# Kernel optimization log

Measured on AMD Instinct MI355X. Metric: run time of the kernel, lower is better.

Reference implementation:

```python
import jax, jax.numpy as jnp
import numpy as np
import math

HIDDEN = 2048
NUM_HEADS = 16
NUM_KV_HEADS = 4
HEAD_DIM = 128
GROUPS = NUM_HEADS // NUM_KV_HEADS
BATCH = 1
SEQ = 4096
THETA = 10000.0


def _rope(x):
    # x: [B, h, S, D], interleaved-pair rotation as in the torch module
    seq = x.shape[2]
    freqs = 1.0 / (THETA ** (jnp.arange(0, HEAD_DIM, 2, dtype=jnp.float32) / HEAD_DIM))  # [D/2]
    angles = jnp.arange(seq, dtype=jnp.float32)[:, None] * freqs[None, :]  # [S, D/2]
    cos = jnp.cos(angles)[None, None]  # [1,1,S,D/2]
    sin = jnp.sin(angles)[None, None]
    x1 = x[..., 0::2]
    x2 = x[..., 1::2]
    # stack along new last axis then flatten -> interleaved layout
    rot = jnp.stack([x1 * cos - x2 * sin, x1 * sin + x2 * cos], axis=-1)
    return rot.reshape(x.shape)


def setup_inputs() -> dict:
    key = jax.random.key(0)
    kx, kq, kk, kv, ko = jax.random.split(key, 5)
    scale = 0.02
    x = jax.random.normal(kx, (BATCH, SEQ, HIDDEN), dtype=jnp.float32)
    Wq = jax.random.normal(kq, (NUM_HEADS * HEAD_DIM, HIDDEN), dtype=jnp.float32) * scale
    Wk = jax.random.normal(kk, (NUM_KV_HEADS * HEAD_DIM, HIDDEN), dtype=jnp.float32) * scale
    Wv = jax.random.normal(kv, (NUM_KV_HEADS * HEAD_DIM, HIDDEN), dtype=jnp.float32) * scale
    Wo = jax.random.normal(ko, (HIDDEN, NUM_HEADS * HEAD_DIM), dtype=jnp.float32) * scale
    return {"x": x, "Wq": Wq, "Wk": Wk, "Wv": Wv, "Wo": Wo}


def reference(x, Wq, Wk, Wv, Wo):
    B, S, _ = x.shape
    q = (x @ Wq.T).reshape(B, S, NUM_HEADS, HEAD_DIM).transpose(0, 2, 1, 3)      # [B,16,S,D]
    k = (x @ Wk.T).reshape(B, S, NUM_KV_HEADS, HEAD_DIM).transpose(0, 2, 1, 3)   # [B,4,S,D]
    v = (x @ Wv.T).reshape(B, S, NUM_KV_HEADS, HEAD_DIM).transpose(0, 2, 1, 3)
    q = _rope(q)
    k = _rope(k)
    # GQA: repeat_interleave KV heads across the group dim
    k = jnp.repeat(k, GROUPS, axis=1)  # [B,16,S,D]
    v = jnp.repeat(v, GROUPS, axis=1)
    scale = 1.0 / math.sqrt(HEAD_DIM)
    scores = jnp.einsum("bhqd,bhkd->bhqk", q, k) * scale  # [B,16,S,S]
    causal = jnp.triu(jnp.ones((S, S), dtype=bool), k=1)
    scores = jnp.where(causal[None, None], jnp.float32(-jnp.inf), scores)
    attn = jax.nn.softmax(scores, axis=-1)
    out = jnp.einsum("bhqk,bhkd->bhqd", attn, v)           # [B,16,S,D]
    out = out.transpose(0, 2, 1, 3).reshape(B, S, NUM_HEADS * HEAD_DIM)
    return out @ Wo.T
```

## Files before the change

kernel.cpp:

```cpp
#include <hip/hip_runtime.h>
#include <hip/hip_bf16.h>

typedef unsigned short u16;
typedef unsigned int u32;
typedef short short8 __attribute__((ext_vector_type(8)));
typedef unsigned short ushort4v __attribute__((ext_vector_type(4)));
typedef float f32x4 __attribute__((ext_vector_type(4)));
typedef float f32x16 __attribute__((ext_vector_type(16)));
typedef u32 u32x4 __attribute__((ext_vector_type(4)));

#define SEQN 4096
#define HID 2048
#define NH 16
#define NKV 4
#define HD 128
#define QDIM 2048
#define KVD 512
#define QKVS 3072

static __device__ __forceinline__ float bf2f(u16 u){
  unsigned x = ((unsigned)u) << 16; float f; __builtin_memcpy(&f, &x, 4); return f;
}
static __device__ __forceinline__ u16 f2bf(float f){
  unsigned x; __builtin_memcpy(&x, &f, 4);
  x += 0x7fffu + ((x >> 16) & 1u);
  return (u16)(x >> 16);
}
static __device__ __forceinline__ u16 f2bfc(float f){
  unsigned x; __builtin_memcpy(&x, &f, 4);
  return (u16)((x + 0x8000u) >> 16);
}
static __device__ __forceinline__ u32 pkr(float a, float b){
  u32 ab, bb; __builtin_memcpy(&ab, &a, 4); __builtin_memcpy(&bb, &b, 4);
  return ((ab + 0x8000u) >> 16) | ((bb + 0x8000u) & 0xffff0000u);
}

#define G1 (SEQN*HID/4)
#define G2 (QDIM*HID/4)
#define G3 (KVD*HID/4)
#define G4 (KVD*HID/4)
#define G5 (HID*QDIM/4)
__global__ __launch_bounds__(256) void cvt5_kernel(const float* __restrict__ x,  const float* __restrict__ Wq,
                                                   const float* __restrict__ Wk, const float* __restrict__ Wv,
                                                   const float* __restrict__ Wo, u16* __restrict__ xb,
                                                   u16* __restrict__ Wqkvb, u16* __restrict__ Wob){
  int g = blockIdx.x * 256 + threadIdx.x;
  const float* src; u16* dst; int off;
  if (g < G1)                { src = x;  dst = xb;    off = g; }
  else if (g < G1+G2)        { src = Wq; dst = Wqkvb; off = g - G1; }
  else if (g < G1+G2+G3)     { src = Wk; dst = Wqkvb + (size_t)QDIM*HID;        off = g - (G1+G2); }
  else if (g < G1+G2+G3+G4)  { src = Wv; dst = Wqkvb + (size_t)(QDIM+KVD)*HID;  off = g - (G1+G2+G3); }
  else if (g < G1+G2+G3+G4+G5){ src = Wo; dst = Wob;  off = g - (G1+G2+G3+G4); }
  else return;
  f32x4 v = ((const f32x4*)src)[off];
  ushort4v o;
  o.x = f2bf(v.x); o.y = f2bf(v.y); o.z = f2bf(v.z); o.w = f2bf(v.w);
  ((ushort4v*)dst)[off] = o;
}

#define ROPE_BLKS (SEQN * (NH + NKV) * 16 / 256)
__global__ __launch_bounds__(256) void prep_kernel(u16* __restrict__ QKVb, u16* __restrict__ VTg){
  __shared__ u16 T[64][72];
  const int bid = blockIdx.x;
  const int tid = threadIdx.x;
  if (bid < ROPE_BLKS){
    int idx = bid * 256 + tid;
    int i8 = idx & 15;
    int rest = idx >> 4;
    int h = rest % (NH + NKV);
    int s = rest / (NH + NKV);
    int col = (h < NH) ? h * HD : QDIM + (h - NH) * HD;
    u16* p = QKVb + (size_t)s * QKVS + col + i8 * 8;
    short8 v = *(const short8*)p;
    short8 o;
#pragma unroll
    for (int j = 0; j < 4; j++){
      int i = i8 * 4 + j;
      float freq = expf(-0.14391156831212788f * (float)i);
      float ang = (float)s * freq;
      float c = cosf(ang), sn = sinf(ang);
      float x1 = bf2f((u16)v[2*j]), x2 = bf2f((u16)v[2*j+1]);
      o[2*j]   = (short)f2bfc(x1 * c - x2 * sn);
      o[2*j+1] = (short)f2bfc(x1 * sn + x2 * c);
    }
    *(short8*)p = o;
  } else {
    const int b2 = bid - ROPE_BLKS;
    const int s0 = (b2 & 63) * 64;
    const int c0 = (b2 >> 6) * 64;
    const int sl = tid & 63, ch = tid >> 6;
    const u16* src = QKVb + QDIM + KVD + (size_t)(s0 + sl) * QKVS + c0 + ch * 16;
    *(short8*)&T[sl][ch * 16]     = *(const short8*)(src);
    *(short8*)&T[sl][ch * 16 + 8] = *(const short8*)(src + 8);
    __syncthreads();
#pragma unroll
    for (int it = 0; it < 16; it++){
      int c = it * 4 + ch;
      VTg[(size_t)(c0 + c) * SEQN + s0 + sl] = T[sl][c];
    }
  }
}

static __device__ __forceinline__ void gload16(const void* g, void* l){
  __builtin_amdgcn_global_load_lds((const __attribute__((address_space(1))) void*)g,
                                   (__attribute__((address_space(3))) void*)l, 16, 0, 0);
}

template<int F32OUT>
__global__ __launch_bounds__(256) void gemm_kernel(const u16* __restrict__ A, const u16* __restrict__ B,
                                                   void* __restrict__ Cout, int M, int N, int Kd, int ldc){
  __shared__ alignas(16) u16 sh[8192];
  u16* As = sh;
  u16* Bs = sh + 4096;
  const int tid = threadIdx.x;
  const int w = tid >> 6, l = tid & 63;
  const int wr = w >> 1, wc = w & 1;
  const int lc = l & 15, lg = l >> 4;
  const int tm = blockIdx.x * 128, tn = blockIdx.y * 128;

  const int srow = w * 32 + (l >> 2);
  const int scol = (l & 3) * 8;
  const u16* Ag = A + (size_t)(tm + srow) * Kd + scol;
  const u16* Bg = B + (size_t)(tn + srow) * Kd + scol;
  u16* As0 = As + (w * 2) * 512;
  u16* Bs0 = Bs + (w * 2) * 512;

  f32x4 acc[4][4] = {};

  for (int k0 = 0; k0 < Kd; k0 += 32){
    gload16(Ag + k0,                    As0);
    gload16(Ag + k0 + (size_t)16 * Kd,  As0 + 512);
    gload16(Bg + k0,                    Bs0);
    gload16(Bg + k0 + (size_t)16 * Kd,  Bs0 + 512);
    __syncthreads();
    short8 a[4], b[4];
#pragma unroll
    for (int mi = 0; mi < 4; mi++) a[mi] = *(const short8*)&As[(wr*64 + mi*16 + lc) * 32 + lg*8];
#pragma unroll
    for (int ni = 0; ni < 4; ni++) b[ni] = *(const short8*)&Bs[(wc*64 + ni*16 + lc) * 32 + lg*8];
#pragma unroll
    for (int mi = 0; mi < 4; mi++)
#pragma unroll
      for (int ni = 0; ni < 4; ni++)
        acc[mi][ni] = __builtin_amdgcn_mfma_f32_16x16x32_bf16(a[mi], b[ni], acc[mi][ni], 0, 0, 0);
    __syncthreads();
  }

  if (F32OUT){
#pragma unroll
    for (int mi = 0; mi < 4; mi++)
#pragma unroll
      for (int ni = 0; ni < 4; ni++)
#pragma unroll
        for (int r = 0; r < 4; r++){
          int row = tm + wr*64 + mi*16 + lg*4 + r;
          int col = tn + wc*64 + ni*16 + lc;
          ((float*)Cout)[(size_t)row * ldc + col] = acc[mi][ni][r];
        }
  } else {
    __syncthreads();
    u16* Ew = sh + w * 1168;
#pragma unroll
    for (int mi = 0; mi < 4; mi++){
#pragma unroll
      for (int ni = 0; ni < 4; ni++)
#pragma unroll
        for (int r = 0; r < 4; r++)
          Ew[(lg * 4 + r) * 73 + ni * 16 + lc] = f2bfc(acc[mi][ni][r]);
#pragma unroll
      for (int pass = 0; pass < 2; pass++){
        int row = pass * 8 + (l >> 3);
        short8 v;
#pragma unroll
        for (int j = 0; j < 8; j++) v[j] = (short)Ew[row * 73 + (l & 7) * 8 + j];
        *(short8*)((u16*)Cout + (size_t)(tm + wr*64 + mi*16 + row) * ldc + tn + wc*64 + (l & 7) * 8) = v;
      }
    }
  }
}

__global__ __launch_bounds__(256, 2) void attn_kernel(const u16* __restrict__ Qg, const u16* __restrict__ Kgb,
                                                      const u16* __restrict__ VTg, u16* __restrict__ Aout,
                                                      u16* __restrict__ PO, float* __restrict__ mP,
                                                      float* __restrict__ LP){
  __shared__ alignas(16) char pool[65536];

  const int pr  = blockIdx.x;
  const int h   = blockIdx.y;
  const int s   = blockIdx.z;
  const int kvh = h >> 2;
  const int tid = threadIdx.x;
  const int w = tid >> 6, l = tid & 63;
  const int q5 = l & 31;
  const int hi = l >> 5;
  const int hi4 = hi * 4;
  const float csc = 0.12751743f;

  const u16* Ksrc[4];
  const u16* Vsrc[4];
#pragma unroll
  for (int i = 0; i < 4; i++){
    int blk = w * 4 + i;
    int row = blk * 4 + (l >> 4);
    int cg  = (l & 15) ^ (row & 15);
    Ksrc[i] = Kgb + (size_t)row * QKVS + kvh * HD + cg * 8;
    int d   = blk * 8 + (l >> 3);
    int cv  = (l & 7) ^ (d & 7);
    Vsrc[i] = VTg + (size_t)(kvh * 128 + d) * SEQN + cv * 8;
  }

  auto issueTile = [&](int b, int kv0){
    char* Ksb = pool + b * 32768;
    char* VTb = Ksb + 16384;
#pragma unroll
    for (int i = 0; i < 4; i++)
      gload16(Ksrc[i] + (size_t)kv0 * QKVS, Ksb + (w * 4 + i) * 1024);
#pragma unroll
    for (int i = 0; i < 4; i++)
      gload16(Vsrc[i] + kv0, VTb + (w * 4 + i) * 1024);
  };

  const int qlo = pr, qhi = 31 - pr;
  int nseg, sq[2], st0[2], st1[2], smode[2];
  if (s == 0){
    nseg = 2;
    sq[0] = qlo; st0[0] = 0;           st1[0] = 2 * pr + 2;   smode[0] = 0;
    sq[1] = qhi; st0[1] = 0;           st1[1] = 31 - 2 * pr;  smode[1] = 1;
  } else {
    nseg = 1;
    sq[0] = qhi; st0[0] = 31 - 2 * pr; st1[0] = 64 - 2 * pr;  smode[0] = 2;
  }

  for (int sg = 0; sg < nseg; sg++){
    const int qt = sq[sg], t0 = st0[sg], t1 = st1[sg], mode = smode[sg];
    const int qbase = qt * 128 + w * 32;
    const int qa    = qbase + q5;

    short8 qf[8];
    {
      const u16* qp = Qg + (size_t)(qbase + q5) * QKVS + h * HD + hi * 8;
#pragma unroll
      for (int k0 = 0; k0 < 8; k0++) qf[k0] = *(const short8*)(qp + k0 * 16);
    }

    f32x16 Ov[4] = {};
    float Lrow = 0.f;
    float ms = -1e30f;

    auto computeTile = [&](int b, int kv0){
      if (kv0 > qbase + 31) return;
      char* Ksb = pool + b * 32768;
      char* VTb = Ksb + 16384;
      f32x16 Sv[2] = {};
#pragma unroll
      for (int k0 = 0; k0 < 8; k0++){
#pragma unroll
        for (int nb = 0; nb < 2; nb++){
          int kvr = nb * 32 + q5;
          short8 kf = *(const short8*)(Ksb + kvr * 256 + (((k0 * 2 + hi) ^ (kvr & 15)) << 4));
          Sv[nb] = __builtin_amdgcn_mfma_f32_32x32x16_bf16(kf, qf[k0], Sv[nb], 0, 0, 0);
        }
      }
      if (kv0 + 63 > qbase){
#pragma unroll
        for (int nb = 0; nb < 2; nb++)
#pragma unroll
          for (int r = 0; r < 16; r++){
            int kva = kv0 + nb * 32 + (r & 3) + 8 * (r >> 2) + hi4;
            if (kva > qa) Sv[nb][r] = -1e30f;
          }
      }
      float tm = fmaxf(Sv[0][0], Sv[0][1]);
#pragma unroll
      for (int nb = 0; nb < 2; nb++)
#pragma unroll
        for (int r = (nb == 0 ? 2 : 0); r < 16; r += 2)
          tm = fmaxf(tm, fmaxf(Sv[nb][r], Sv[nb][r + 1]));
      tm = fmaxf(tm, __shfl_xor(tm, 32));
      float tms = tm * csc;
      if (!__all(tms - ms <= 8.f)){
        float nms = fmaxf(ms, tms);
        float al = __builtin_amdgcn_exp2f(ms - nms);
        ms = nms;
        Lrow *= al;
#pragma unroll
        for (int nb = 0; nb < 4; nb++)
#pragma unroll
          for (int r = 0; r < 16; r++) Ov[nb][r] *= al;
      }
      float ts0 = 0.f, ts1 = 0.f;
#pragma unroll
      for (int nb = 0; nb < 2; nb++)
#pragma unroll
        for (int r = 0; r < 16; r += 2){
          float p0 = __builtin_amdgcn_exp2f(__builtin_fmaf(Sv[nb][r],     csc, -ms));
          float p1 = __builtin_amdgcn_exp2f(__builtin_fmaf(Sv[nb][r + 1], csc, -ms));
          Sv[nb][r] = p0; Sv[nb][r + 1] = p1;
          ts0 += p0; ts1 += p1;
        }
      float ts = ts0 + ts1;
      ts += __shfl_xor(ts, 32);
      Lrow += ts;
#pragma unroll
      for (int kc = 0; kc < 4; kc++){
        const int nb = kc >> 1, rb = (kc & 1) * 8;
        u32 Aw = pkr(Sv[nb][rb + 0], Sv[nb][rb + 1]);
        u32 Bw = pkr(Sv[nb][rb + 2], Sv[nb][rb + 3]);
        u32 Cw = pkr(Sv[nb][rb + 4], Sv[nb][rb + 5]);
        u32 Dw = pkr(Sv[nb][rb + 6], Sv[nb][rb + 7]);
        u32 sAw = __shfl_xor(Aw, 32);
        u32 sBw = __shfl_xor(Bw, 32);
        u32 sCw = __shfl_xor(Cw, 32);
        u32 sDw = __shfl_xor(Dw, 32);
        u32 w0 = hi ? sCw : Aw;
        u32 w1 = hi ? sDw : Bw;
        u32 w2 = hi ? Cw : sAw;
        u32 w3 = hi ? Dw : sBw;
        u32x4 pw4 = {w0, w1, w2, w3};
        short8 pf = *(short8*)&pw4;
#pragma unroll
        for (int nbd = 0; nbd < 4; nbd++){
          int drow = nbd * 32 + q5;
          short8 vf = *(const short8*)(VTb + drow * 128 + (((kc * 2 + hi) ^ (drow & 7)) << 4));
          Ov[nbd] = __builtin_amdgcn_mfma_f32_32x32x16_bf16(vf, pf, Ov[nbd], 0, 0, 0);
        }
      }
    };

    __syncthreads();
    issueTile(0, t0 * 64);
    __syncthreads();
    int cur = 0;
    for (int t = t0; t < t1; t++){
      if (t + 1 < t1) issueTile(cur ^ 1, (t + 1) * 64);
      computeTile(cur, t * 64);
      __syncthreads();
      cur ^= 1;
    }

    u16* Ew = (u16*)(pool + w * 8704);
    float rl = (mode == 0) ? (1.f / Lrow) : 1.f;
#pragma unroll
    for (int nbd = 0; nbd < 4; nbd++)
#pragma unroll
      for (int r = 0; r < 16; r += 2){
        int d = nbd * 32 + (r & 3) + 8 * (r >> 2) + hi4;
        u32 wpk = pkr(Ov[nbd][r] * rl, Ov[nbd][r + 1] * rl);
        *(u32*)((char*)Ew + q5 * 272 + d * 2) = wpk;
      }
    if (mode == 0){
#pragma unroll
      for (int pass = 0; pass < 8; pass++){
        int q2 = pass * 4 + (l >> 4);
        short8 ov = *(const short8*)((char*)Ew + q2 * 272 + (l & 15) * 16);
        *(short8*)(Aout + (size_t)(qbase + q2) * QDIM + h * HD + (l & 15) * 8) = ov;
      }
    } else {
      const int p = mode - 1;
      u16* dstb = PO + ((size_t)((p * 16 + pr) * NH + h) * 128) * 128;
#pragma unroll
      for (int pass = 0; pass < 8; pass++){
        int q2 = pass * 4 + (l >> 4);
        short8 ov = *(const short8*)((char*)Ew + q2 * 272 + (l & 15) * 16);
        *(short8*)(dstb + (size_t)(w * 32 + q2) * 128 + (l & 15) * 8) = ov;
      }
      if (hi == 0){
        int idx = ((p * 16 + pr) * NH + h) * 128 + w * 32 + q5;
        mP[idx] = ms;
        LP[idx] = Lrow;
      }
    }
  }
}

__global__ __launch_bounds__(256) void combine_kernel(const u16* __restrict__ PO, const float* __restrict__ mP,
                                                      const float* __restrict__ LP, u16* __restrict__ Aout){
  const int pr = blockIdx.x;
  const int h  = blockIdx.y;
  const int tid = threadIdx.x;
  const int r  = tid >> 1;
  const int dh = (tid & 1) * 64;
  const int qhi = 31 - pr;
  const int idx0 = ((0 * 16 + pr) * NH + h) * 128 + r;
  const int idx1 = ((1 * 16 + pr) * NH + h) * 128 + r;
  float m0 = mP[idx0], m1 = mP[idx1];
  float L0 = LP[idx0], L1 = LP[idx1];
  float M = fmaxf(m0, m1);
  float a0 = __builtin_amdgcn_exp2f(m0 - M);
  float a1 = __builtin_amdgcn_exp2f(m1 - M);
  float rl = 1.f / (L0 * a0 + L1 * a1);
  const u16* o0 = PO + (size_t)idx0 * 128 + dh;
  const u16* o1 = PO + (size_t)idx1 * 128 + dh;
  u16* dst = Aout + (size_t)(qhi * 128 + r) * QDIM + h * HD + dh;
#pragma unroll
  for (int ch = 0; ch < 8; ch++){
    short8 v0 = *(const short8*)(o0 + ch * 8);
    short8 v1 = *(const short8*)(o1 + ch * 8);
    u32x4 ow;
#pragma unroll
    for (int j = 0; j < 4; j++){
      float e0 = (bf2f((u16)v0[2*j])   * a0 + bf2f((u16)v1[2*j])   * a1) * rl;
      float e1 = (bf2f((u16)v0[2*j+1]) * a0 + bf2f((u16)v1[2*j+1]) * a1) * rl;
      ow[j] = pkr(e0, e1);
    }
    *(u32x4*)(dst + ch * 8) = ow;
  }
}

extern "C" void kernel_launch(void* const* d_in, const int* in_sizes, int n_in,
                              void* d_out, int out_size, void* d_ws, size_t ws_size,
                              hipStream_t stream){
  const float* x  = (const float*)d_in[0];
  const float* Wq = (const float*)d_in[1];
  const float* Wk = (const float*)d_in[2];
  const float* Wv = (const float*)d_in[3];
  const float* Wo = (const float*)d_in[4];

  char* p = (char*)d_ws;
  u16* xb    = (u16*)p; p += (size_t)SEQN * HID * 2;
  u16* Wqkvb = (u16*)p; p += (size_t)QKVS * HID * 2;
  u16* Wob   = (u16*)p; p += (size_t)HID * QDIM * 2;
  u16* QKVb  = (u16*)p; p += (size_t)SEQN * QKVS * 2;
  u16* Ab    = (u16*)p; p += (size_t)SEQN * QDIM * 2;
  u16* VTg   = (u16*)p; p += (size_t)SEQN * KVD * 2;
  u16* PO    = (u16*)p; p += (size_t)2 * 16 * NH * 128 * 128 * 2;
  float* mP  = (float*)p; p += (size_t)2 * 16 * NH * 128 * 4;
  float* LP  = (float*)p; p += (size_t)2 * 16 * NH * 128 * 4;

  const int totg = G1 + G2 + G3 + G4 + G5;
  cvt5_kernel<<<(totg + 255) / 256, 256, 0, stream>>>(x, Wq, Wk, Wv, Wo, xb, Wqkvb, Wob);

  gemm_kernel<0><<<dim3(SEQN/128, QKVS/128), 256, 0, stream>>>(xb, Wqkvb, QKVb, SEQN, QKVS, HID, QKVS);

  prep_kernel<<<ROPE_BLKS + (SEQN/64) * (KVD/64), 256, 0, stream>>>(QKVb, VTg);

  attn_kernel<<<dim3(16, NH, 2), 256, 0, stream>>>(QKVb, QKVb + QDIM, VTg, Ab, PO, mP, LP);
  combine_kernel<<<dim3(16, NH), 256, 0, stream>>>(PO, mP, LP, Ab);

  gemm_kernel<1><<<dim3(SEQN/128, HID/128), 256, 0, stream>>>(Ab, Wob, d_out, SEQN, HID, QDIM, HID);
}
```

Measured before the change: 254.4 us.

## Halve attention KV tile to 32 rows to fit three blocks per CU

Shrinks the K/V tile from 64 to 32 keys, which halves the shared-memory pool and the score registers so the launch bound can go from 2 to 3 blocks per CU. Global source pointers become 32-bit byte offsets to save registers, and the V swizzle and segment tile ranges are rescaled to match. The aim is higher occupancy to hide latency, at the cost of twice as many loop iterations and barriers and more online-softmax rescale checks per key.

```diff
diff --git a/kernel.cpp b/kernel.cpp
--- a/kernel.cpp
+++ b/kernel.cpp
@@ -179,11 +179,11 @@
   }
 }
 
-__global__ __launch_bounds__(256, 2) void attn_kernel(const u16* __restrict__ Qg, const u16* __restrict__ Kgb,
+__global__ __launch_bounds__(256, 3) void attn_kernel(const u16* __restrict__ Qg, const u16* __restrict__ Kgb,
                                                       const u16* __restrict__ VTg, u16* __restrict__ Aout,
                                                       u16* __restrict__ PO, float* __restrict__ mP,
                                                       float* __restrict__ LP){
-  __shared__ alignas(16) char pool[65536];
+  __shared__ alignas(16) char pool[34816];
 
   const int pr  = blockIdx.x;
   const int h   = blockIdx.y;
@@ -196,39 +196,38 @@
   const int hi4 = hi * 4;
   const float csc = 0.12751743f;
 
-  const u16* Ksrc[4];
-  const u16* Vsrc[4];
-#pragma unroll
-  for (int i = 0; i < 4; i++){
-    int blk = w * 4 + i;
+  u32 Koff[2], Voff[2];
+#pragma unroll
+  for (int i = 0; i < 2; i++){
+    int blk = w * 2 + i;
     int row = blk * 4 + (l >> 4);
     int cg  = (l & 15) ^ (row & 15);
-    Ksrc[i] = Kgb + (size_t)row * QKVS + kvh * HD + cg * 8;
-    int d   = blk * 8 + (l >> 3);
-    int cv  = (l & 7) ^ (d & 7);
-    Vsrc[i] = VTg + (size_t)(kvh * 128 + d) * SEQN + cv * 8;
+    Koff[i] = (u32)((row * QKVS + kvh * HD + cg * 8) * 2);
+    int d   = blk * 16 + (l >> 2);
+    int cv  = (l & 3) ^ (d & 3);
+    Voff[i] = (u32)(((kvh * 128 + d) * SEQN + cv * 8) * 2);
   }
 
   auto issueTile = [&](int b, int kv0){
-    char* Ksb = pool + b * 32768;
-    char* VTb = Ksb + 16384;
-#pragma unroll
-    for (int i = 0; i < 4; i++)
-      gload16(Ksrc[i] + (size_t)kv0 * QKVS, Ksb + (w * 4 + i) * 1024);
-#pragma unroll
-    for (int i = 0; i < 4; i++)
-      gload16(Vsrc[i] + kv0, VTb + (w * 4 + i) * 1024);
+    char* Ksb = pool + b * 16384;
+    char* VTb = Ksb + 8192;
+#pragma unroll
+    for (int i = 0; i < 2; i++)
+      gload16((const char*)Kgb + (size_t)Koff[i] + (size_t)kv0 * (QKVS * 2), Ksb + (w * 2 + i) * 1024);
+#pragma unroll
+    for (int i = 0; i < 2; i++)
+      gload16((const char*)VTg + (size_t)Voff[i] + (size_t)kv0 * 2, VTb + (w * 2 + i) * 1024);
   };
 
   const int qlo = pr, qhi = 31 - pr;
   int nseg, sq[2], st0[2], st1[2], smode[2];
   if (s == 0){
     nseg = 2;
-    sq[0] = qlo; st0[0] = 0;           st1[0] = 2 * pr + 2;   smode[0] = 0;
-    sq[1] = qhi; st0[1] = 0;           st1[1] = 31 - 2 * pr;  smode[1] = 1;
+    sq[0] = qlo; st0[0] = 0;            st1[0] = 4 * pr + 4;    smode[0] = 0;
+    sq[1] = qhi; st0[1] = 0;            st1[1] = 62 - 4 * pr;   smode[1] = 1;
   } else {
     nseg = 1;
-    sq[0] = qhi; st0[0] = 31 - 2 * pr; st1[0] = 64 - 2 * pr;  smode[0] = 2;
+    sq[0] = qhi; st0[0] = 62 - 4 * pr;  st1[0] = 128 - 4 * pr;  smode[0] = 2;
   }
 
   for (int sg = 0; sg < nseg; sg++){
@@ -249,33 +248,25 @@
 
     auto computeTile = [&](int b, int kv0){
       if (kv0 > qbase + 31) return;
-      char* Ksb = pool + b * 32768;
-      char* VTb = Ksb + 16384;
-      f32x16 Sv[2] = {};
+      char* Ksb = pool + b * 16384;
+      char* VTb = Ksb + 8192;
+      f32x16 Sv = {};
 #pragma unroll
       for (int k0 = 0; k0 < 8; k0++){
-#pragma unroll
-        for (int nb = 0; nb < 2; nb++){
-          int kvr = nb * 32 + q5;
-          short8 kf = *(const short8*)(Ksb + kvr * 256 + (((k0 * 2 + hi) ^ (kvr & 15)) << 4));
-          Sv[nb] = __builtin_amdgcn_mfma_f32_32x32x16_bf16(kf, qf[k0], Sv[nb], 0, 0, 0);
+        short8 kf = *(const short8*)(Ksb + q5 * 256 + (((k0 * 2 + hi) ^ (q5 & 15)) << 4));
+        Sv = __builtin_amdgcn_mfma_f32_32x32x16_bf16(kf, qf[k0], Sv, 0, 0, 0);
+      }
+      if (kv0 + 31 > qbase){
+#pragma unroll
+        for (int r = 0; r < 16; r++){
+          int kva = kv0 + (r & 3) + 8 * (r >> 2) + hi4;
+          if (kva > qa) Sv[r] = -1e30f;
         }
       }
-      if (kv0 + 63 > qbase){
-#pragma unroll
-        for (int nb = 0; nb < 2; nb++)
-#pragma unroll
-          for (int r = 0; r < 16; r++){
-            int kva = kv0 + nb * 32 + (r & 3) + 8 * (r >> 2) + hi4;
-            if (kva > qa) Sv[nb][r] = -1e30f;
-          }
-      }
-      float tm = fmaxf(Sv[0][0], Sv[0][1]);
-#pragma unroll
-      for (int nb = 0; nb < 2; nb++)
-#pragma unroll
-        for (int r = (nb == 0 ? 2 : 0); r < 16; r += 2)
-          tm = fmaxf(tm, fmaxf(Sv[nb][r], Sv[nb][r + 1]));
+      float tm = fmaxf(Sv[0], Sv[1]);
+#pragma unroll
+      for (int r = 2; r < 16; r += 2)
+        tm = fmaxf(tm, fmaxf(Sv[r], Sv[r + 1]));
       tm = fmaxf(tm, __shfl_xor(tm, 32));
       float tms = tm * csc;
       if (!__all(tms - ms <= 8.f)){
@@ -290,24 +281,22 @@
       }
       float ts0 = 0.f, ts1 = 0.f;
 #pragma unroll
-      for (int nb = 0; nb < 2; nb++)
-#pragma unroll
-        for (int r = 0; r < 16; r += 2){
-          float p0 = __builtin_amdgcn_exp2f(__builtin_fmaf(Sv[nb][r],     csc, -ms));
-          float p1 = __builtin_amdgcn_exp2f(__builtin_fmaf(Sv[nb][r + 1], csc, -ms));
-          Sv[nb][r] = p0; Sv[nb][r + 1] = p1;
-          ts0 += p0; ts1 += p1;
-        }
+      for (int r = 0; r < 16; r += 2){
+        float p0 = __builtin_amdgcn_exp2f(__builtin_fmaf(Sv[r],     csc, -ms));
+        float p1 = __builtin_amdgcn_exp2f(__builtin_fmaf(Sv[r + 1], csc, -ms));
+        Sv[r] = p0; Sv[r + 1] = p1;
+        ts0 += p0; ts1 += p1;
+      }
       float ts = ts0 + ts1;
       ts += __shfl_xor(ts, 32);
       Lrow += ts;
 #pragma unroll
-      for (int kc = 0; kc < 4; kc++){
-        const int nb = kc >> 1, rb = (kc & 1) * 8;
-        u32 Aw = pkr(Sv[nb][rb + 0], Sv[nb][rb + 1]);
-        u32 Bw = pkr(Sv[nb][rb + 2], Sv[nb][rb + 3]);
-        u32 Cw = pkr(Sv[nb][rb + 4], Sv[nb][rb + 5]);
-        u32 Dw = pkr(Sv[nb][rb + 6], Sv[nb][rb + 7]);
+      for (int kc = 0; kc < 2; kc++){
+        const int rb = kc * 8;
+        u32 Aw = pkr(Sv[rb + 0], Sv[rb + 1]);
+        u32 Bw = pkr(Sv[rb + 2], Sv[rb + 3]);
+        u32 Cw = pkr(Sv[rb + 4], Sv[rb + 5]);
+        u32 Dw = pkr(Sv[rb + 6], Sv[rb + 7]);
         u32 sAw = __shfl_xor(Aw, 32);
         u32 sBw = __shfl_xor(Bw, 32);
         u32 sCw = __shfl_xor(Cw, 32);
@@ -321,19 +310,19 @@
 #pragma unroll
         for (int nbd = 0; nbd < 4; nbd++){
           int drow = nbd * 32 + q5;
-          short8 vf = *(const short8*)(VTb + drow * 128 + (((kc * 2 + hi) ^ (drow & 7)) << 4));
+          short8 vf = *(const short8*)(VTb + drow * 64 + (((kc * 2 + hi) ^ (drow & 3)) << 4));
           Ov[nbd] = __builtin_amdgcn_mfma_f32_32x32x16_bf16(vf, pf, Ov[nbd], 0, 0, 0);
         }
       }
     };
 
     __syncthreads();
-    issueTile(0, t0 * 64);
+    issueTile(0, t0 * 32);
     __syncthreads();
     int cur = 0;
     for (int t = t0; t < t1; t++){
-      if (t + 1 < t1) issueTile(cur ^ 1, (t + 1) * 64);
-      computeTile(cur, t * 64);
+      if (t + 1 < t1) issueTile(cur ^ 1, (t + 1) * 32);
+      computeTile(cur, t * 32);
       __syncthreads();
       cur ^= 1;
     }
```

After: 268.7 us. +5.6%, slower.

## Multi-stage LDS pipeline with XOR swizzle in projection GEMM

Applied to the files above, without the earlier changes.

Turns the GEMM main loop from a single-buffered load/sync/compute cycle into a 4-slot LDS ring with two stages of prefetch in flight. Manual vmcnt waits and one barrier per iteration replace the two __syncthreads. The A/B tiles are stored with an XOR column swizzle to cut LDS bank conflicts on the MFMA fragment reads. LDS use grows from 16KB to 64KB per block, which may lower occupancy. Reusing slots relies on the waitcnt and barrier ordering being correct.

```diff
diff --git a/kernel.cpp b/kernel.cpp
--- a/kernel.cpp
+++ b/kernel.cpp
@@ -109,41 +109,62 @@
 template<int F32OUT>
 __global__ __launch_bounds__(256) void gemm_kernel(const u16* __restrict__ A, const u16* __restrict__ B,
                                                    void* __restrict__ Cout, int M, int N, int Kd, int ldc){
-  __shared__ alignas(16) u16 sh[8192];
-  u16* As = sh;
-  u16* Bs = sh + 4096;
+  __shared__ alignas(16) u16 sh[32768];
   const int tid = threadIdx.x;
   const int w = tid >> 6, l = tid & 63;
   const int wr = w >> 1, wc = w & 1;
   const int lc = l & 15, lg = l >> 4;
   const int tm = blockIdx.x * 128, tn = blockIdx.y * 128;
 
-  const int srow = w * 32 + (l >> 2);
-  const int scol = (l & 3) * 8;
-  const u16* Ag = A + (size_t)(tm + srow) * Kd + scol;
-  const u16* Bg = B + (size_t)(tn + srow) * Kd + scol;
-  u16* As0 = As + (w * 2) * 512;
-  u16* Bs0 = Bs + (w * 2) * 512;
+  const u16* src[4];
+#pragma unroll
+  for (int i = 0; i < 4; i++){
+    int blk = w * 4 + i;
+    int row = (blk & 7) * 16 + (l >> 2);
+    int cs  = (l & 3) ^ (row & 3);
+    src[i] = (blk < 8) ? (A + (size_t)(tm + row) * Kd + cs * 8)
+                       : (B + (size_t)(tn + row) * Kd + cs * 8);
+  }
+
+  auto issueStage = [&](int slot, int t){
+    char* base = (char*)sh + slot * 16384;
+    int k0 = t * 32;
+#pragma unroll
+    for (int i = 0; i < 4; i++)
+      gload16(src[i] + k0, base + (w * 4 + i) * 1024);
+  };
 
   f32x4 acc[4][4] = {};
-
-  for (int k0 = 0; k0 < Kd; k0 += 32){
-    gload16(Ag + k0,                    As0);
-    gload16(Ag + k0 + (size_t)16 * Kd,  As0 + 512);
-    gload16(Bg + k0,                    Bs0);
-    gload16(Bg + k0 + (size_t)16 * Kd,  Bs0 + 512);
-    __syncthreads();
+  const int T = Kd / 32;
+
+  issueStage(0, 0);
+  issueStage(1, 1);
+
+  for (int t = 0; t < T; t++){
+    if (t + 2 < T) issueStage((t + 2) & 3, t + 2);
+    if (t + 2 < T)      asm volatile("s_waitcnt vmcnt(8)" ::: "memory");
+    else if (t + 1 < T) asm volatile("s_waitcnt vmcnt(4)" ::: "memory");
+    else                asm volatile("s_waitcnt vmcnt(0)" ::: "memory");
+    __builtin_amdgcn_s_barrier();
+    __builtin_amdgcn_sched_barrier(0);
+
+    const char* base = (const char*)sh + (t & 3) * 16384;
     short8 a[4], b[4];
 #pragma unroll
-    for (int mi = 0; mi < 4; mi++) a[mi] = *(const short8*)&As[(wr*64 + mi*16 + lc) * 32 + lg*8];
-#pragma unroll
-    for (int ni = 0; ni < 4; ni++) b[ni] = *(const short8*)&Bs[(wc*64 + ni*16 + lc) * 32 + lg*8];
+    for (int mi = 0; mi < 4; mi++){
+      int row = wr * 64 + mi * 16 + lc;
+      a[mi] = *(const short8*)(base + row * 64 + ((lg ^ (row & 3)) * 16));
+    }
+#pragma unroll
+    for (int ni = 0; ni < 4; ni++){
+      int row = wc * 64 + ni * 16 + lc;
+      b[ni] = *(const short8*)(base + 8192 + row * 64 + ((lg ^ (row & 3)) * 16));
+    }
 #pragma unroll
     for (int mi = 0; mi < 4; mi++)
 #pragma unroll
       for (int ni = 0; ni < 4; ni++)
         acc[mi][ni] = __builtin_amdgcn_mfma_f32_16x16x32_bf16(a[mi], b[ni], acc[mi][ni], 0, 0, 0);
-    __syncthreads();
   }
 
   if (F32OUT){
```

New measurement: 238.2 us, median of 3. -6.4%, faster.
